# Kernel optimization log

Hardware: AMD Instinct MI355X
Metric: run time of the kernel (lower is better)

Reference implementation:

```python
import jax, jax.numpy as jnp
import numpy as np

HIDDEN = 2048
HEADS = 16
HEAD_DIM = HIDDEN // HEADS
BATCH = 2
SEQ = 2048


def setup_inputs() -> dict:
    key = jax.random.key(0)
    ks = jax.random.split(key, 9)
    s = 0.02
    return {
        "x": jax.random.normal(ks[0], (BATCH, SEQ, HIDDEN), dtype=jnp.float32),
        "Wq": jax.random.normal(ks[1], (HIDDEN, HIDDEN), dtype=jnp.float32) * s,
        "bq": jax.random.normal(ks[2], (HIDDEN,), dtype=jnp.float32) * s,
        "Wk": jax.random.normal(ks[3], (HIDDEN, HIDDEN), dtype=jnp.float32) * s,
        "bk": jax.random.normal(ks[4], (HIDDEN,), dtype=jnp.float32) * s,
        "Wv": jax.random.normal(ks[5], (HIDDEN, HIDDEN), dtype=jnp.float32) * s,
        "bv": jax.random.normal(ks[6], (HIDDEN,), dtype=jnp.float32) * s,
        "Wo": jax.random.normal(ks[7], (HIDDEN, HIDDEN), dtype=jnp.float32) * s,
        "bo": jax.random.normal(ks[8], (HIDDEN,), dtype=jnp.float32) * s,
    }


def reference(x, Wq, bq, Wk, bk, Wv, bv, Wo, bo):
    B, S, H = x.shape
    # Linear layers: y = x @ W.T + b (torch nn.Linear convention, W:[out,in])
    q = x @ Wq.T + bq
    k = x @ Wk.T + bk
    v = x @ Wv.T + bv
    # [B, S, H] -> [B, nH, S, hd]
    def split_heads(t):
        return t.reshape(B, S, HEADS, HEAD_DIM).transpose(0, 2, 1, 3)
    q, k, v = split_heads(q), split_heads(k), split_heads(v)
    scale = 1.0 / (HEAD_DIM ** 0.5)
    # NOTE: original module applies NO causal mask despite its name; be faithful.
    scores = jnp.einsum('bhqd,bhkd->bhqk', q, k) * scale
    probs = jax.nn.softmax(scores, axis=-1)
    attn = jnp.einsum('bhqk,bhkd->bhqd', probs, v)
    attn = attn.transpose(0, 2, 1, 3).reshape(B, S, H)
    return attn @ Wo.T + bo
```

## Files before the change

kernel.cpp:

```cpp
#include <hip/hip_runtime.h>
#include <hip/hip_bf16.h>
#include <stdint.h>

typedef __bf16 bf16_t;
typedef __attribute__((ext_vector_type(8))) __bf16 bf16x8;
typedef __attribute__((ext_vector_type(4))) float floatx4;
typedef __attribute__((ext_vector_type(16))) float f32x16;
typedef __attribute__((ext_vector_type(2))) int i32x2;

typedef __attribute__((address_space(1))) const unsigned int gu32_t;
typedef __attribute__((address_space(3))) unsigned int lu32_t;

__device__ __forceinline__ void async16(const void* g, void* l) {
    __builtin_amdgcn_global_load_lds((gu32_t*)g, (lu32_t*)l, 16, 0, 0);
}

__device__ __forceinline__ uint32_t pack2(float lo, float hi) {
    union { bf16_t h[2]; uint32_t u; } cv;
    cv.h[0] = (bf16_t)lo; cv.h[1] = (bf16_t)hi;
    return cv.u;
}

__global__ __launch_bounds__(256) void cvt_f32_bf16(const float* __restrict__ in,
                                                    bf16_t* __restrict__ out) {
    int i = (blockIdx.x * 256 + threadIdx.x) * 8;
    float4 a = *(const float4*)(in + i);
    float4 b = *(const float4*)(in + i + 4);
    bf16x8 v;
    v[0] = (bf16_t)a.x; v[1] = (bf16_t)a.y; v[2] = (bf16_t)a.z; v[3] = (bf16_t)a.w;
    v[4] = (bf16_t)b.x; v[5] = (bf16_t)b.y; v[6] = (bf16_t)b.z; v[7] = (bf16_t)b.w;
    *(bf16x8*)(out + i) = v;
}

__global__ __launch_bounds__(256) void cvt4_f32_bf16(const float* __restrict__ w0,
                                                     const float* __restrict__ w1,
                                                     const float* __restrict__ w2,
                                                     const float* __restrict__ w3,
                                                     bf16_t* __restrict__ out,
                                                     int elems) {
    const float* srcs[4] = {w0, w1, w2, w3};
    const float* in = srcs[blockIdx.y];
    bf16_t* o = out + (size_t)blockIdx.y * elems;
    int i = (blockIdx.x * 256 + threadIdx.x) * 8;
    float4 a = *(const float4*)(in + i);
    float4 b = *(const float4*)(in + i + 4);
    bf16x8 v;
    v[0] = (bf16_t)a.x; v[1] = (bf16_t)a.y; v[2] = (bf16_t)a.z; v[3] = (bf16_t)a.w;
    v[4] = (bf16_t)b.x; v[5] = (bf16_t)b.y; v[6] = (bf16_t)b.z; v[7] = (bf16_t)b.w;
    *(bf16x8*)(o + i) = v;
}

template <bool OUT_F32, bool BIAS_ROW>
__global__ __launch_bounds__(256) void gemm_bt(const bf16_t* __restrict__ A,
                                               const bf16_t* __restrict__ B,
                                               const float* __restrict__ bias,
                                               const float* __restrict__ bias2,
                                               int nsplit, float scaleA, float scaleB,
                                               float* __restrict__ Cf,
                                               bf16_t* __restrict__ Cb,
                                               int M, int N, int K, int ldc) {
    __shared__ bf16_t As[128 * 64];
    __shared__ bf16_t Bs[128 * 64];
    const int tid = threadIdx.x;
    const int wave = tid >> 6, lane = tid & 63;
    const int quad = lane >> 4, l16 = lane & 15;
    const int wm = (wave >> 1) * 64, wn = (wave & 1) * 64;
    const int tm = blockIdx.x * 128, tn = blockIdx.y * 128;

    floatx4 acc[4][4];
#pragma unroll
    for (int i = 0; i < 4; ++i)
#pragma unroll
        for (int j = 0; j < 4; ++j) acc[i][j] = floatx4{0.f, 0.f, 0.f, 0.f};

    const bf16_t* Abase = A + (size_t)tm * K;
    const bf16_t* Bbase = B + (size_t)tn * K;
    const int sw = l16 & 7;

    for (int kk = 0; kk < K; kk += 64) {
#pragma unroll
        for (int it = 0; it < 4; ++it) {
            int chunk = it * 256 + tid;
            int r = chunk >> 3, c = chunk & 7;
            int c2 = c ^ (r & 7);
            async16(Abase + r * K + kk + c2 * 8, As + (it * 256 + wave * 64) * 8);
            async16(Bbase + r * K + kk + c2 * 8, Bs + (it * 256 + wave * 64) * 8);
        }
        __syncthreads();
#pragma unroll
        for (int ks = 0; ks < 2; ++ks) {
            bf16x8 af[4], bf[4];
#pragma unroll
            for (int mt = 0; mt < 4; ++mt)
                af[mt] = *(const bf16x8*)(As + (wm + mt * 16 + l16) * 64 +
                                          ((ks * 4 + quad) ^ sw) * 8);
#pragma unroll
            for (int nt = 0; nt < 4; ++nt)
                bf[nt] = *(const bf16x8*)(Bs + (wn + nt * 16 + l16) * 64 +
                                          ((ks * 4 + quad) ^ sw) * 8);
#pragma unroll
            for (int mt = 0; mt < 4; ++mt)
#pragma unroll
                for (int nt = 0; nt < 4; ++nt)
                    acc[mt][nt] = __builtin_amdgcn_mfma_f32_16x16x32_bf16(af[mt], bf[nt],
                                                                          acc[mt][nt], 0, 0, 0);
        }
        __syncthreads();
    }
#pragma unroll
    for (int mt = 0; mt < 4; ++mt)
#pragma unroll
        for (int nt = 0; nt < 4; ++nt)
#pragma unroll
            for (int r = 0; r < 4; ++r) {
                int row = tm + wm + mt * 16 + quad * 4 + r;
                int col = tn + wn + nt * 16 + l16;
                float bv = BIAS_ROW ? bias[row]
                                    : (col < nsplit ? bias[col] : bias2[col - nsplit]);
                float v = acc[mt][nt][r] + bv;
                if (!BIAS_ROW) v *= (col < nsplit ? scaleA : scaleB);
                if (OUT_F32) Cf[(size_t)row * ldc + col] = v;
                else Cb[(size_t)row * ldc + col] = (bf16_t)v;
            }
}

#define KELEMS (64 * 128)
#define VELEMS (128 * 64)
__global__ __launch_bounds__(256, 2) void flash_attn(const bf16_t* __restrict__ Qp,
                                                     const bf16_t* __restrict__ Kp,
                                                     const bf16_t* __restrict__ Vt,
                                                     bf16_t* __restrict__ O) {
    __shared__ bf16_t smem[2 * KELEMS + 2 * VELEMS];
    const int tid = threadIdx.x;
    const int wv = tid >> 6, lane = tid & 63;
    const int hi = lane >> 5, l32 = lane & 31;
    const int wq = wv >> 1, wk = wv & 1;
    const int LD = 4096, T = 4096, S = 2048, HO = 2048;

    const int gid = blockIdx.x;
    const int kq = gid >> 3;
    const int qt = kq & 31;
    const int grp = (gid & 7) + 8 * (kq >> 5);
    const int hd = grp & 15, bt = grp >> 4;

    const int qrow0 = bt * S + qt * 64;
    const int krow0 = bt * S;
    const int hoff = hd * 128;
    const int sw7 = l32 & 7;
    const int swK = l32 & 15;

    bf16x8 qf[8];
    const bf16_t* qptr = Qp + (size_t)(qrow0 + wq * 32 + l32) * LD + hoff + hi * 8;
#pragma unroll
    for (int ks = 0; ks < 8; ++ks) qf[ks] = *(const bf16x8*)(qptr + ks * 16);

    float l_i = 0.f;
    f32x16 Oacc[4];
#pragma unroll
    for (int dt = 0; dt < 4; ++dt)
#pragma unroll
        for (int r = 0; r < 16; ++r) Oacc[dt][r] = 0.f;

    auto stageK = [&](int kt, int b) {
        int kb = krow0 + kt * 64;
        bf16_t* Ks = smem + b * KELEMS;
#pragma unroll
        for (int it = 0; it < 4; ++it) {
            int chunk = it * 256 + tid;
            int r = chunk >> 4, c = chunk & 15;
            int c2 = c ^ (r & 15);
            async16(Kp + (size_t)(kb + r) * LD + hoff + c2 * 8, Ks + chunk * 8);
        }
    };
    auto stageV = [&](int kt, int b) {
        int kb = krow0 + kt * 64;
        bf16_t* Vts = smem + 2 * KELEMS + b * VELEMS;
#pragma unroll
        for (int it = 0; it < 4; ++it) {
            int chunk = it * 256 + tid;
            int r = chunk >> 3, c = chunk & 7;
            int c2 = c ^ (r & 7);
            async16(Vt + (size_t)(hoff + r) * T + kb + c2 * 8, Vts + chunk * 8);
        }
    };

    auto pv = [&](const uint32_t* pk, int vb) {
        const bf16_t* Vts = smem + 2 * KELEMS + vb * VELEMS;
#pragma unroll
        for (int s = 0; s < 2; ++s) {
            i32x2 s02 = __builtin_amdgcn_permlane32_swap((int)pk[4 * s + 0],
                                                         (int)pk[4 * s + 2], false, false);
            i32x2 s13 = __builtin_amdgcn_permlane32_swap((int)pk[4 * s + 1],
                                                         (int)pk[4 * s + 3], false, false);
            union { uint32_t u[4]; bf16x8 v; } w;
            w.u[0] = (uint32_t)s02[0];
            w.u[1] = (uint32_t)s13[0];
            w.u[2] = (uint32_t)s02[1];
            w.u[3] = (uint32_t)s13[1];
#pragma unroll
            for (int dt = 0; dt < 4; ++dt) {
                bf16x8 a = *(const bf16x8*)(Vts + (dt * 32 + l32) * 64 +
                                            ((4 * wk + 2 * s + hi) ^ sw7) * 8);
                Oacc[dt] = __builtin_amdgcn_mfma_f32_32x32x16_bf16(a, w.v, Oacc[dt], 0, 0, 0);
            }
        }
    };

    uint32_t pkPrev[8];
    stageK(0, 0);
    stageV(0, 0);
    for (int kt = 0; kt < 32; ++kt) {
        const int cur = kt & 1;
        __syncthreads();
        if (kt + 1 < 32) stageK(kt + 1, cur ^ 1);

        const bf16_t* Ks = smem + cur * KELEMS;

        f32x16 sf0, sf1;
#pragma unroll
        for (int r = 0; r < 16; ++r) { sf0[r] = 0.f; sf1[r] = 0.f; }
#pragma unroll
        for (int ks = 0; ks < 4; ++ks) {
            bf16x8 a0 = *(const bf16x8*)(Ks + (wk * 32 + l32) * 128 +
                                         ((2 * ks + hi) ^ swK) * 8);
            bf16x8 a1 = *(const bf16x8*)(Ks + (wk * 32 + l32) * 128 +
                                         ((2 * (ks + 4) + hi) ^ swK) * 8);
            sf0 = __builtin_amdgcn_mfma_f32_32x32x16_bf16(a0, qf[ks], sf0, 0, 0, 0);
            sf1 = __builtin_amdgcn_mfma_f32_32x32x16_bf16(a1, qf[ks + 4], sf1, 0, 0, 0);
        }

        if (kt > 0) pv(pkPrev, cur ^ 1);

        __syncthreads();
        if (kt + 1 < 32) stageV(kt + 1, cur ^ 1);

        float rs0 = 0.f, rs1 = 0.f;
#pragma unroll
        for (int a4 = 0; a4 < 4; ++a4) {
            float p0 = exp2f(sf0[4 * a4 + 0] + sf1[4 * a4 + 0]);
            float p1 = exp2f(sf0[4 * a4 + 1] + sf1[4 * a4 + 1]);
            float p2 = exp2f(sf0[4 * a4 + 2] + sf1[4 * a4 + 2]);
            float p3 = exp2f(sf0[4 * a4 + 3] + sf1[4 * a4 + 3]);
            rs0 += p0 + p1;
            rs1 += p2 + p3;
            pkPrev[a4 * 2 + 0] = pack2(p0, p1);
            pkPrev[a4 * 2 + 1] = pack2(p2, p3);
        }
        l_i += rs0 + rs1;
    }

    pv(pkPrev, 1);

    __syncthreads();
    l_i += __shfl_xor(l_i, 32);
    float* ml = (float*)smem;
    if (hi == 0) ml[wv * 32 + l32] = l_i;
    __syncthreads();
    float linv = 1.0f / (l_i + ml[(wv ^ 1) * 32 + l32]);
    __syncthreads();

    float* Op = (float*)smem;
    if (wk == 1) {
#pragma unroll
        for (int dt = 0; dt < 4; ++dt)
#pragma unroll
            for (int r = 0; r < 16; ++r) {
                int d = dt * 32 + (r & 3) + 8 * (r >> 2) + 4 * hi;
                Op[(wq * 128 + d) * 32 + l32] = Oacc[dt][r];
            }
    }
    __syncthreads();
    if (wk == 0) {
#pragma unroll
        for (int dt = 0; dt < 4; ++dt)
#pragma unroll
            for (int r = 0; r < 16; ++r) {
                int d = dt * 32 + (r & 3) + 8 * (r >> 2) + 4 * hi;
                Oacc[dt][r] = (Oacc[dt][r] + Op[(wq * 128 + d) * 32 + l32]) * linv;
            }
    }
    __syncthreads();

    if (wk == 0) {
        uint32_t* Os = (uint32_t*)smem + wq * 2048;
#pragma unroll
        for (int dt = 0; dt < 4; ++dt)
#pragma unroll
            for (int a4 = 0; a4 < 4; ++a4) {
                uint32_t q0 = pack2(Oacc[dt][4 * a4 + 0], Oacc[dt][4 * a4 + 1]);
                uint32_t q1 = pack2(Oacc[dt][4 * a4 + 2], Oacc[dt][4 * a4 + 3]);
                int d2 = 16 * dt + 4 * a4 + 2 * hi;
                Os[l32 * 64 + ((d2 + 2 * l32) & 63)] = q0;
                Os[l32 * 64 + ((d2 + 1 + 2 * l32) & 63)] = q1;
            }
#pragma unroll
        for (int r = 0; r < 32; ++r) {
            uint32_t v = Os[r * 64 + ((lane + 2 * r) & 63)];
            uint32_t* orow = (uint32_t*)(O + (size_t)(qrow0 + wq * 32 + r) * HO + hoff);
            orow[lane] = v;
        }
    }
}

extern "C" void kernel_launch(void* const* d_in, const int* in_sizes, int n_in,
                              void* d_out, int out_size, void* d_ws, size_t ws_size,
                              hipStream_t stream) {
    const float* x  = (const float*)d_in[0];
    const float* Wq = (const float*)d_in[1];
    const float* bq = (const float*)d_in[2];
    const float* Wk = (const float*)d_in[3];
    const float* bk = (const float*)d_in[4];
    const float* Wv = (const float*)d_in[5];
    const float* bv = (const float*)d_in[6];
    const float* Wo = (const float*)d_in[7];
    const float* bo = (const float*)d_in[8];
    float* out = (float*)d_out;

    const int T = 4096;
    const int H = 2048;
    const float SL2E = 0.088388347688f * 1.44269504089f;
    bf16_t* ws  = (bf16_t*)d_ws;
    bf16_t* xb  = ws;
    bf16_t* wqb = xb  + (size_t)T * H;
    bf16_t* wkb = wqb + (size_t)H * H;
    bf16_t* wvb = wkb + (size_t)H * H;
    bf16_t* wob = wvb + (size_t)H * H;
    bf16_t* QKb = wob + (size_t)H * H;
    bf16_t* Vtb = QKb + (size_t)T * 2 * H;
    bf16_t* Ab  = Vtb + (size_t)H * T;
    size_t need = (size_t)(Ab + (size_t)T * H - ws) * sizeof(bf16_t);
    if (ws_size < need) return;

    cvt_f32_bf16<<<T * H / 2048, 256, 0, stream>>>(x, xb);
    cvt4_f32_bf16<<<dim3(H * H / 2048, 4), 256, 0, stream>>>(Wq, Wk, Wv, Wo, wqb, H * H);

    dim3 gqk(T / 128, 4096 / 128);
    gemm_bt<false, false><<<gqk, 256, 0, stream>>>(xb, wqb, bq, bk, H, SL2E, 1.0f,
                                                   nullptr, QKb, T, 4096, H, 4096);
    dim3 gv(H / 128, T / 128);
    gemm_bt<false, true><<<gv, 256, 0, stream>>>(wvb, xb, bv, nullptr, 0, 1.0f, 1.0f,
                                                 nullptr, Vtb, H, T, H, T);

    flash_attn<<<1024, 256, 0, stream>>>(QKb, QKb + H, Vtb, Ab);

    dim3 go(T / 128, H / 128);
    gemm_bt<true, false><<<go, 256, 0, stream>>>(Ab, wob, bo, nullptr, H, 1.0f, 1.0f,
                                                 out, nullptr, T, H, H, H);
}
```

Baseline: 419.8 us.

## Add 256x256-tile 512-thread GEMM for QK projection and raise MFMA priority

Result: faster. 399.7 us (-4.8%).

```diff
diff --git a/kernel.cpp b/kernel.cpp
--- a/kernel.cpp
+++ b/kernel.cpp
@@ -124,6 +124,128 @@
             }
 }
 
+template <bool OUT_F32>
+__global__ __launch_bounds__(512, 2) void gemm256(const bf16_t* __restrict__ A,
+                                                  const bf16_t* __restrict__ B,
+                                                  const float* __restrict__ bias,
+                                                  const float* __restrict__ bias2,
+                                                  int nsplit, float scaleA, float scaleB,
+                                                  float* __restrict__ Cf,
+                                                  bf16_t* __restrict__ Cb,
+                                                  int M, int N, int K, int ldc) {
+    __shared__ bf16_t As[2][256 * 64];
+    __shared__ bf16_t Bs[2][256 * 64];
+    const int tid = threadIdx.x;
+    const int wave = tid >> 6, lane = tid & 63;
+    const int quad = lane >> 4, l16 = lane & 15;
+    const int wr = wave >> 2, wc = wave & 3;
+    const int nbx = M >> 8, nby = N >> 8;
+    const int nwg = nbx * nby;
+    const int xcd = blockIdx.x & 7, idx = blockIdx.x >> 3;
+    const int per = nwg >> 3;
+    const int wg = xcd * per + idx;
+    const int tm = (wg % nbx) * 256, tn = (wg / nbx) * 256;
+
+    floatx4 acc[8][4];
+#pragma unroll
+    for (int i = 0; i < 8; ++i)
+#pragma unroll
+        for (int j = 0; j < 4; ++j) acc[i][j] = floatx4{0.f, 0.f, 0.f, 0.f};
+
+    const bf16_t* Abase = A + (size_t)tm * K;
+    const bf16_t* Bbase = B + (size_t)tn * K;
+    const int sw = l16 & 7;
+    const int NT = K >> 6;
+
+    auto stageA = [&](int kk, int b) {
+#pragma unroll
+        for (int it = 0; it < 4; ++it) {
+            int chunk = it * 512 + tid;
+            int r = chunk >> 3, c = chunk & 7;
+            int c2 = c ^ (r & 7);
+            async16(Abase + (size_t)r * K + kk + c2 * 8, As[b] + chunk * 8);
+        }
+    };
+    auto stageB = [&](int kk, int b) {
+#pragma unroll
+        for (int it = 0; it < 4; ++it) {
+            int chunk = it * 512 + tid;
+            int r = chunk >> 3, c = chunk & 7;
+            int c2 = c ^ (r & 7);
+            async16(Bbase + (size_t)r * K + kk + c2 * 8, Bs[b] + chunk * 8);
+        }
+    };
+
+    stageA(0, 0);
+    stageB(0, 0);
+    asm volatile("s_waitcnt vmcnt(0)" ::: "memory");
+    __builtin_amdgcn_s_barrier();
+    __builtin_amdgcn_sched_barrier(0);
+
+    for (int t = 0; t < NT; ++t) {
+        const int cur = t & 1;
+        const bf16_t* Asb = As[cur];
+        const bf16_t* Bsb = Bs[cur];
+        const int nk = (t + 1) << 6;
+        const bool more = (t + 1 < NT);
+#pragma unroll
+        for (int p = 0; p < 4; ++p) {
+            const int mh = p >> 1, nh = p & 1;
+            bf16x8 af[4][2], bf[2][2];
+#pragma unroll
+            for (int mt = 0; mt < 4; ++mt) {
+                int row = wr * 128 + mh * 64 + mt * 16 + l16;
+#pragma unroll
+                for (int ks = 0; ks < 2; ++ks)
+                    af[mt][ks] = *(const bf16x8*)(Asb + row * 64 + ((ks * 4 + quad) ^ sw) * 8);
+            }
+#pragma unroll
+            for (int nt = 0; nt < 2; ++nt) {
+                int col = wc * 64 + nh * 32 + nt * 16 + l16;
+#pragma unroll
+                for (int ks = 0; ks < 2; ++ks)
+                    bf[nt][ks] = *(const bf16x8*)(Bsb + col * 64 + ((ks * 4 + quad) ^ sw) * 8);
+            }
+            if (more) {
+                if (p == 0) stageA(nk, cur ^ 1);
+                else if (p == 1) stageB(nk, cur ^ 1);
+            }
+            __builtin_amdgcn_s_barrier();
+            asm volatile("s_waitcnt lgkmcnt(0)" ::: "memory");
+            __builtin_amdgcn_sched_barrier(0);
+            __builtin_amdgcn_s_setprio(1);
+#pragma unroll
+            for (int ks = 0; ks < 2; ++ks)
+#pragma unroll
+                for (int mt = 0; mt < 4; ++mt)
+#pragma unroll
+                    for (int nt = 0; nt < 2; ++nt)
+                        acc[mh * 4 + mt][nh * 2 + nt] =
+                            __builtin_amdgcn_mfma_f32_16x16x32_bf16(
+                                af[mt][ks], bf[nt][ks], acc[mh * 4 + mt][nh * 2 + nt], 0, 0, 0);
+            __builtin_amdgcn_s_setprio(0);
+            if (p == 3 && more)
+                asm volatile("s_waitcnt vmcnt(0)" ::: "memory");
+            __builtin_amdgcn_s_barrier();
+            __builtin_amdgcn_sched_barrier(0);
+        }
+    }
+
+#pragma unroll
+    for (int am = 0; am < 8; ++am)
+#pragma unroll
+        for (int an = 0; an < 4; ++an)
+#pragma unroll
+            for (int r = 0; r < 4; ++r) {
+                int row = tm + wr * 128 + (am >> 2) * 64 + (am & 3) * 16 + quad * 4 + r;
+                int col = tn + wc * 64 + (an >> 1) * 32 + (an & 1) * 16 + l16;
+                float bv = col < nsplit ? bias[col] : bias2[col - nsplit];
+                float v = (acc[am][an][r] + bv) * (col < nsplit ? scaleA : scaleB);
+                if (OUT_F32) Cf[(size_t)row * ldc + col] = v;
+                else Cb[(size_t)row * ldc + col] = (bf16_t)v;
+            }
+}
+
 #define KELEMS (64 * 128)
 #define VELEMS (128 * 64)
 __global__ __launch_bounds__(256, 2) void flash_attn(const bf16_t* __restrict__ Qp,
@@ -186,6 +308,7 @@
 
     auto pv = [&](const uint32_t* pk, int vb) {
         const bf16_t* Vts = smem + 2 * KELEMS + vb * VELEMS;
+        __builtin_amdgcn_s_setprio(1);
 #pragma unroll
         for (int s = 0; s < 2; ++s) {
             i32x2 s02 = __builtin_amdgcn_permlane32_swap((int)pk[4 * s + 0],
@@ -204,6 +327,7 @@
                 Oacc[dt] = __builtin_amdgcn_mfma_f32_32x32x16_bf16(a, w.v, Oacc[dt], 0, 0, 0);
             }
         }
+        __builtin_amdgcn_s_setprio(0);
     };
 
     uint32_t pkPrev[8];
@@ -219,6 +343,7 @@
         f32x16 sf0, sf1;
 #pragma unroll
         for (int r = 0; r < 16; ++r) { sf0[r] = 0.f; sf1[r] = 0.f; }
+        __builtin_amdgcn_s_setprio(1);
 #pragma unroll
         for (int ks = 0; ks < 4; ++ks) {
             bf16x8 a0 = *(const bf16x8*)(Ks + (wk * 32 + l32) * 128 +
@@ -228,6 +353,7 @@
             sf0 = __builtin_amdgcn_mfma_f32_32x32x16_bf16(a0, qf[ks], sf0, 0, 0, 0);
             sf1 = __builtin_amdgcn_mfma_f32_32x32x16_bf16(a1, qf[ks + 4], sf1, 0, 0, 0);
         }
+        __builtin_amdgcn_s_setprio(0);
 
         if (kt > 0) pv(pkPrev, cur ^ 1);
 
@@ -334,9 +460,9 @@
     cvt_f32_bf16<<<T * H / 2048, 256, 0, stream>>>(x, xb);
     cvt4_f32_bf16<<<dim3(H * H / 2048, 4), 256, 0, stream>>>(Wq, Wk, Wv, Wo, wqb, H * H);
 
-    dim3 gqk(T / 128, 4096 / 128);
-    gemm_bt<false, false><<<gqk, 256, 0, stream>>>(xb, wqb, bq, bk, H, SL2E, 1.0f,
-                                                   nullptr, QKb, T, 4096, H, 4096);
+    gemm256<false><<<(T / 256) * (4096 / 256), 512, 0, stream>>>(
+        xb, wqb, bq, bk, H, SL2E, 1.0f, nullptr, QKb, T, 4096, H, 4096);
+
     dim3 gv(H / 128, T / 128);
     gemm_bt<false, true><<<gv, 256, 0, stream>>>(wvb, xb, bv, nullptr, 0, 1.0f, 1.0f,
                                                  nullptr, Vtb, H, T, H, T);
```
